# Performance work log

Hardware: AMD Instinct MI355X
Metric: run time of the kernel (lower is better)

Reference implementation:

```python
import jax, jax.numpy as jnp
import numpy as np

EPS = 1e-8
N = 1024          # number of points
C = 16            # channels per layer
RBF_LOW, RBF_HIGH, RBF_COUNT = 0.0, 3.5, 32


def _rand(key, shape, scale=0.1):
    return scale * jax.random.normal(key, shape, dtype=jnp.float32)


def setup_inputs() -> dict:
    key = jax.random.key(0)
    ks = jax.random.split(key, 20)
    R = RBF_COUNT
    return {
        'points':   jax.random.normal(ks[0], (N, 3), dtype=jnp.float32),
        # layer 1: 2 radial filters (0->0 and 0->1), output_dim = 1 input channel
        'l1_W1':    _rand(ks[1],  (2, R, R)),
        'l1_B1':    _rand(ks[2],  (2, R)),
        'l1_W2':    _rand(ks[3],  (2, R, 1)),
        'l1_B2':    _rand(ks[4],  (2, 1)),
        'l1_si0_w': _rand(ks[5],  (C, 1)),
        'l1_si0_b': _rand(ks[6],  (C,)),
        'l1_si1_w': _rand(ks[7],  (C, 1)),
        'l1_nl_b':  _rand(ks[8],  (C,)),
        # layer 2: 5 radial filters (0->0, 0->1, 1->0, 1->1 id, 1->1 levi-civita)
        'l2_W1':    _rand(ks[9],  (5, R, R)),
        'l2_B1':    _rand(ks[10], (5, R)),
        'l2_W2':    _rand(ks[11], (5, R, C)),
        'l2_B2':    _rand(ks[12], (5, C)),
        'l2_si0_w': _rand(ks[13], (C, 2 * C)),
        'l2_si0_b': _rand(ks[14], (C,)),
        'l2_si1_w': _rand(ks[15], (C, 3 * C)),
        'l2_nl_b':  _rand(ks[16], (C,)),
        # readout
        'fc_w':     _rand(ks[17], (C, 8)),
        'fc_b':     _rand(ks[18], (8,)),
    }


def _eijk():
    e = np.zeros((3, 3, 3), dtype=np.float32)
    e[0, 1, 2] = e[1, 2, 0] = e[2, 0, 1] = 1.0
    e[0, 2, 1] = e[2, 1, 0] = e[1, 0, 2] = -1.0
    return jnp.asarray(e)


def _norm_eps(x, axis, keepdims=False):
    # norm_with_epsilon: sqrt(max(sum(x^2), EPS))
    return jnp.sqrt(jnp.maximum(jnp.sum(x * x, axis=axis, keepdims=keepdims), EPS))


def _radial(rbf, w1, b1, w2, b2):
    # R(): two-layer relu MLP on rbf features -> [N, N, F]
    h = jax.nn.relu(rbf @ w1 + b1)
    return h @ w2 + b2


def _geometry(points):
    rij = points[:, None, :] - points[None, :, :]          # [N,N,3]
    ss = jnp.sum(rij * rij, axis=-1)                        # [N,N]
    mask0 = ss < EPS                                        # dij == 0 (diagonal)
    dij = jnp.where(mask0, 0.0, jnp.sqrt(jnp.where(mask0, 1.0, ss)))
    centers = jnp.linspace(RBF_LOW, RBF_HIGH, RBF_COUNT, dtype=jnp.float32)
    gamma = jnp.float32(RBF_COUNT / (RBF_HIGH - RBF_LOW))
    rbf = jnp.exp(-gamma * (dij[..., None] - centers) ** 2)  # [N,N,RBF]
    unit = rij / _norm_eps(rij, axis=-1, keepdims=True)       # unit_vectors
    return rbf, unit, mask0


def _F1(rad, unit, mask0):
    # F_1: mask radial where dij==0, multiply by unit vectors -> [N,N,F,3]
    mr = jnp.where(mask0[..., None], 0.0, rad)
    return mr[..., None] * unit[:, :, None, :]


def _nonlinearity(x0, x1, b1):
    # degree-0: pointwise elu; degree-1: norm nonlinearity x * elu(|x|+b)/|x|
    x0 = jax.nn.elu(x0)
    n = _norm_eps(x1, axis=-1)                              # [N,C]
    x1 = x1 * (jax.nn.elu(n + b1) / n)[..., None]
    return x0, x1


def reference(points, l1_W1, l1_B1, l1_W2, l1_B2, l1_si0_w, l1_si0_b, l1_si1_w,
              l1_nl_b, l2_W1, l2_B1, l2_W2, l2_B2, l2_si0_w, l2_si0_b, l2_si1_w,
              l2_nl_b, fc_w, fc_b):
    rbf, unit, mask0 = _geometry(points)
    eijk = _eijk().astype(points.dtype)
    n_pts = points.shape[0]
    x0 = jnp.ones((n_pts, 1, 1), dtype=points.dtype)        # degree-0 input [N,1,1]

    # ---- layer 1: only degree-0 input -> (0->0) and (0->1) filters ----
    r00 = _radial(rbf, l1_W1[0], l1_B1[0], l1_W2[0], l1_B2[0])
    out0 = jnp.einsum('abf,bfi->afi', r00, x0)              # filter_0
    F1a = _F1(_radial(rbf, l1_W1[1], l1_B1[1], l1_W2[1], l1_B2[1]), unit, mask0)
    out1 = jnp.einsum('abfi,bf->afi', F1a, x0[..., 0])
    x0 = jnp.einsum('afi,gf->agi', out0, l1_si0_w) + l1_si0_b[:, None]
    x1 = jnp.einsum('afi,gf->agi', out1, l1_si1_w)
    x0, x1 = _nonlinearity(x0, x1, l1_nl_b)                 # [N,C,1], [N,C,3]

    # ---- layer 2: degree-0 and degree-1 inputs -> 5 filters ----
    rads = [_radial(rbf, l2_W1[i], l2_B1[i], l2_W2[i], l2_B2[i]) for i in range(5)]
    c00 = jnp.einsum('abf,bfi->afi', rads[0], x0)                          # 0x0->0
    c01 = jnp.einsum('abfi,bf->afi', _F1(rads[1], unit, mask0), x0[..., 0])  # 0x1->1
    c10 = jnp.einsum('abfj,bfj->af', _F1(rads[2], unit, mask0), x1)[..., None]  # 1x1->0
    c11 = jnp.einsum('abf,bfi->afi', rads[3], x1)                          # 1x0->1
    c11x = jnp.einsum('ijk,abfj,bfk->afi', eijk, _F1(rads[4], unit, mask0), x1)  # 1x1->1
    cat0 = jnp.concatenate([c00, c10], axis=-2)             # [N,2C,1]
    cat1 = jnp.concatenate([c01, c11, c11x], axis=-2)       # [N,3C,3]
    x0 = jnp.einsum('afi,gf->agi', cat0, l2_si0_w) + l2_si0_b[:, None]
    x1 = jnp.einsum('afi,gf->agi', cat1, l2_si1_w)
    x0, x1 = _nonlinearity(x0, x1, l2_nl_b)

    # ---- readout: invariant degree-0 features, mean-pool over points ----
    g = jnp.mean(x0[..., 0], axis=0)                        # [C]
    return g @ fc_w + fc_b                                  # [num_classes]
```

## Files before the change

### kernel.cpp

```cpp
#include <hip/hip_runtime.h>
#include <hip/hip_bf16.h>
#include <math.h>

#define NP 1024
#define R 32
#define C 16
#define GAMMA (32.0f/3.5f)
#define DC (3.5f/31.0f)

typedef __attribute__((ext_vector_type(8))) short bf16x8;
typedef __attribute__((ext_vector_type(4))) float f32x4;

__device__ __forceinline__ short tobf(float x){
    __hip_bfloat16 h = __float2bfloat16(x);
    return __builtin_bit_cast(short, h);
}
__device__ __forceinline__ float frombf(short s){
    __hip_bfloat16 h = __builtin_bit_cast(__hip_bfloat16, s);
    return __bfloat162float(h);
}
__device__ __forceinline__ unsigned pack2bf(float a, float b){
    const unsigned lo = (unsigned short)tobf(a);
    const unsigned hi = (unsigned short)tobf(b);
    return lo | (hi << 16);
}
__device__ __forceinline__ float eluf(float x){ return x > 0.f ? x : expm1f(x); }

__device__ __forceinline__ f32x4 mfma16(bf16x8 a, bf16x8 b, f32x4 c){
    return __builtin_amdgcn_mfma_f32_16x16x32_bf16(a, b, c, 0, 0, 0);
}

template<int STRIDE>
__device__ __forceinline__ void load_bfrag(const float* __restrict__ src, int q, int n,
                                           bf16x8& hi, bf16x8& lo){
    #pragma unroll
    for (int jj = 0; jj < 8; jj++){
        const float w = src[(q*8+jj)*STRIDE + n];
        const short h = tobf(w);
        hi[jj] = h;
        lo[jj] = tobf(w - frombf(h));
    }
}

__global__ __launch_bounds__(256) void k_layer1(
    const float* __restrict__ points,
    const float* __restrict__ W1, const float* __restrict__ B1,
    const float* __restrict__ W2, const float* __restrict__ B2,
    float* __restrict__ out0, float* __restrict__ out1)
{
    __shared__ float sS0[4][32];
    __shared__ float sT[4][32][3];
    __shared__ float sUp[4][3];

    const int tid  = threadIdx.x;
    const int lane = tid & 63;
    const int wv   = tid >> 6;
    const int l16  = lane & 15;
    const int q    = lane >> 4;
    const int a    = blockIdx.x;
    const float pax = points[a*3+0], pay = points[a*3+1], paz = points[a*3+2];

    bf16x8 w1hi[2][2], w1lo[2][2];
    float  b1v[2][2];
    #pragma unroll
    for (int fi = 0; fi < 2; fi++)
        #pragma unroll
        for (int nt = 0; nt < 2; nt++){
            load_bfrag<R>(W1 + fi*R*R, q, nt*16 + l16, w1hi[fi][nt], w1lo[fi][nt]);
            b1v[fi][nt] = B1[fi*R + nt*16 + l16];
        }

    float s0a[2] = {0.f, 0.f};
    float T[2][3] = {};
    float upx = 0.f, upy = 0.f, upz = 0.f;

    for (int bt = 0; bt < 16; bt++){
        const int bA = bt*64 + wv*16 + l16;
        const float rx = pax - points[bA*3+0];
        const float ry = pay - points[bA*3+1];
        const float rz = paz - points[bA*3+2];
        const float ss = rx*rx + ry*ry + rz*rz;
        const float dij = sqrtf(ss);
        const float inv = 1.0f / sqrtf(fmaxf(ss, 1e-8f));
        const float ux = rx*inv, uy = ry*inv, uz = rz*inv;
        upx += ux; upy += uy; upz += uz;

        bf16x8 afrag;
        #pragma unroll
        for (int jj = 0; jj < 8; jj++){
            const float t = dij - (float)(q*8+jj)*DC;
            afrag[jj] = tobf(__expf(-GAMMA*t*t));
        }

        float uxr[4], uyr[4], uzr[4];
        #pragma unroll
        for (int r4 = 0; r4 < 4; r4++){
            const int sl = q*4 + r4;
            uxr[r4] = __shfl(ux, sl, 16);
            uyr[r4] = __shfl(uy, sl, 16);
            uzr[r4] = __shfl(uz, sl, 16);
        }

        #pragma unroll
        for (int nt = 0; nt < 2; nt++){
            f32x4 c = {b1v[0][nt], b1v[0][nt], b1v[0][nt], b1v[0][nt]};
            c = mfma16(afrag, w1hi[0][nt], c);
            c = mfma16(afrag, w1lo[0][nt], c);
            s0a[nt] += fmaxf(c[0],0.f)+fmaxf(c[1],0.f)+fmaxf(c[2],0.f)+fmaxf(c[3],0.f);
        }
        #pragma unroll
        for (int nt = 0; nt < 2; nt++){
            f32x4 c = {b1v[1][nt], b1v[1][nt], b1v[1][nt], b1v[1][nt]};
            c = mfma16(afrag, w1hi[1][nt], c);
            c = mfma16(afrag, w1lo[1][nt], c);
            #pragma unroll
            for (int r4 = 0; r4 < 4; r4++){
                const float h = fmaxf(c[r4], 0.f);
                T[nt][0] = fmaf(h, uxr[r4], T[nt][0]);
                T[nt][1] = fmaf(h, uyr[r4], T[nt][1]);
                T[nt][2] = fmaf(h, uzr[r4], T[nt][2]);
            }
        }
    }

    #pragma unroll
    for (int nt = 0; nt < 2; nt++){
        s0a[nt] += __shfl_down(s0a[nt], 32, 64);
        s0a[nt] += __shfl_down(s0a[nt], 16, 64);
        #pragma unroll
        for (int i = 0; i < 3; i++){
            T[nt][i] += __shfl_down(T[nt][i], 32, 64);
            T[nt][i] += __shfl_down(T[nt][i], 16, 64);
        }
    }
    #pragma unroll
    for (int off = 32; off > 0; off >>= 1){
        upx += __shfl_down(upx, off, 64);
        upy += __shfl_down(upy, off, 64);
        upz += __shfl_down(upz, off, 64);
    }
    if (lane < 16){
        sS0[wv][lane]      = s0a[0];
        sS0[wv][16 + lane] = s0a[1];
        #pragma unroll
        for (int i = 0; i < 3; i++){
            sT[wv][lane][i]      = T[0][i];
            sT[wv][16 + lane][i] = T[1][i];
        }
    }
    if (lane == 0){ sUp[wv][0] = upx; sUp[wv][1] = upy; sUp[wv][2] = upz; }
    __syncthreads();
    if (tid == 0){
        float o0 = 0.f;
        for (int j = 0; j < R; j++){
            const float S = sS0[0][j] + sS0[1][j] + sS0[2][j] + sS0[3][j];
            o0 = fmaf(S, W2[j], o0);
        }
        out0[a] = o0 + (float)NP * B2[0];
        for (int i = 0; i < 3; i++){
            float t = 0.f;
            for (int j = 0; j < R; j++){
                const float Tj = sT[0][j][i] + sT[1][j][i] + sT[2][j][i] + sT[3][j][i];
                t = fmaf(Tj, W2[R + j], t);
            }
            const float Ui = 0.25f * (sUp[0][i] + sUp[1][i] + sUp[2][i] + sUp[3][i]);
            out1[a*3+i] = t + B2[1] * Ui;
        }
    }
}

__global__ __launch_bounds__(256) void k_point1(
    const float* __restrict__ out0, const float* __restrict__ out1,
    const float* __restrict__ si0_w, const float* __restrict__ si0_b,
    const float* __restrict__ si1_w, const float* __restrict__ nl_b,
    float* __restrict__ x0g, float* __restrict__ x1s)
{
    const int b = blockIdx.x*256 + threadIdx.x;
    if (b >= NP) return;
    const float o0 = out0[b];
    const float o1x = out1[b*3+0], o1y = out1[b*3+1], o1z = out1[b*3+2];
    #pragma unroll
    for (int g = 0; g < C; g++){
        x0g[b*C+g] = eluf(fmaf(o0, si0_w[g], si0_b[g]));
        const float w = si1_w[g];
        const float tx = o1x*w, ty = o1y*w, tz = o1z*w;
        const float n = sqrtf(fmaxf(tx*tx + ty*ty + tz*tz, 1e-8f));
        const float sc = eluf(n + nl_b[g]) / n;
        x1s[0*NP*C + b*C+g] = tx*sc;
        x1s[1*NP*C + b*C+g] = ty*sc;
        x1s[2*NP*C + b*C+g] = tz*sc;
    }
}

__global__ __launch_bounds__(256) void k_layer2(
    const float* __restrict__ points,
    const float* __restrict__ W1, const float* __restrict__ B1,
    const float* __restrict__ W2, const float* __restrict__ B2,
    const float* __restrict__ x0g, const float* __restrict__ x1s,
    float* __restrict__ c00, float* __restrict__ c10)
{
    __shared__ __align__(16) short sH[4][2][16*40];
    __shared__ float sRed[4][2][16];

    const int tid  = threadIdx.x;
    const int lane = tid & 63;
    const int wv   = tid >> 6;
    const int l16  = lane & 15;
    const int q    = lane >> 4;
    const int a    = blockIdx.x;
    const float pax = points[a*3+0], pay = points[a*3+1], paz = points[a*3+2];

    bf16x8 w1hi[2][2], w1lo[2][2], w2hi[2], w2lo[2];
    float  b1v[2][2], b2v[2];
    #pragma unroll
    for (int fi = 0; fi < 2; fi++){
        const int fx = (fi == 0) ? 0 : 2;
        #pragma unroll
        for (int nt = 0; nt < 2; nt++){
            load_bfrag<R>(W1 + fx*R*R, q, 2*l16 + nt, w1hi[fi][nt], w1lo[fi][nt]);
            b1v[fi][nt] = B1[fx*R + 2*l16 + nt];
        }
        load_bfrag<C>(W2 + fx*R*C, q, l16, w2hi[fi], w2lo[fi]);
        b2v[fi] = B2[fx*C + l16];
    }

    float acc0 = 0.f, acc1 = 0.f;
    short* sH0 = sH[wv][0];
    short* sH1 = sH[wv][1];

    for (int bt = 0; bt < 16; bt++){
        const int bA = bt*64 + wv*16 + l16;
        const float rx = pax - points[bA*3+0];
        const float ry = pay - points[bA*3+1];
        const float rz = paz - points[bA*3+2];
        const float ss = rx*rx + ry*ry + rz*rz;
        const float dij = sqrtf(ss);
        const float inv = 1.0f / sqrtf(fmaxf(ss, 1e-8f));
        const float ux = rx*inv, uy = ry*inv, uz = rz*inv;

        float uxr[4], uyr[4], uzr[4];
        #pragma unroll
        for (int r4 = 0; r4 < 4; r4++){
            const int sl = q*4 + r4;
            uxr[r4] = __shfl(ux, sl, 16);
            uyr[r4] = __shfl(uy, sl, 16);
            uzr[r4] = __shfl(uz, sl, 16);
        }

        const int rb = (bt*64 + wv*16 + q*4)*C + l16;
        float x0v[4], udv[4];
        #pragma unroll
        for (int r4 = 0; r4 < 4; r4++){
            x0v[r4] = x0g[rb + r4*C];
            const float v0 = x1s[0*NP*C + rb + r4*C];
            const float v1 = x1s[1*NP*C + rb + r4*C];
            const float v2 = x1s[2*NP*C + rb + r4*C];
            udv[r4] = uxr[r4]*v0 + uyr[r4]*v1 + uzr[r4]*v2;
        }

        bf16x8 afrag;
        #pragma unroll
        for (int jj = 0; jj < 8; jj++){
            const float t = dij - (float)(q*8+jj)*DC;
            afrag[jj] = tobf(__expf(-GAMMA*t*t));
        }

        #pragma unroll
        for (int fi = 0; fi < 2; fi++){
            f32x4 c0 = {b1v[fi][0], b1v[fi][0], b1v[fi][0], b1v[fi][0]};
            c0 = mfma16(afrag, w1hi[fi][0], c0);
            c0 = mfma16(afrag, w1lo[fi][0], c0);
            f32x4 c1 = {b1v[fi][1], b1v[fi][1], b1v[fi][1], b1v[fi][1]};
            c1 = mfma16(afrag, w1hi[fi][1], c1);
            c1 = mfma16(afrag, w1lo[fi][1], c1);
            short* sHf = (fi == 0) ? sH0 : sH1;
            #pragma unroll
            for (int r4 = 0; r4 < 4; r4++){
                const unsigned p = pack2bf(fmaxf(c0[r4], 0.f), fmaxf(c1[r4], 0.f));
                *(unsigned*)&sHf[(q*4+r4)*40 + 2*l16] = p;
            }
        }
        asm volatile("s_waitcnt lgkmcnt(0)" ::: "memory");
        #pragma unroll
        for (int fi = 0; fi < 2; fi++){
            const short* sHf = (fi == 0) ? sH0 : sH1;
            const bf16x8 hf = *(const bf16x8*)(sHf + l16*40 + q*8);
            f32x4 d = {0.f, 0.f, 0.f, 0.f};
            d = mfma16(hf, w2hi[fi], d);
            d = mfma16(hf, w2lo[fi], d);
            #pragma unroll
            for (int r4 = 0; r4 < 4; r4++){
                const float v = d[r4] + b2v[fi];
                if (fi == 0) acc0 = fmaf(v, x0v[r4], acc0);
                else         acc1 = fmaf(v, udv[r4], acc1);
            }
        }
    }

    acc0 += __shfl_down(acc0, 32, 64); acc0 += __shfl_down(acc0, 16, 64);
    acc1 += __shfl_down(acc1, 32, 64); acc1 += __shfl_down(acc1, 16, 64);
    if (lane < 16){ sRed[wv][0][lane] = acc0; sRed[wv][1][lane] = acc1; }
    __syncthreads();
    if (tid < 16)
        c00[a*C + tid] = sRed[0][0][tid] + sRed[1][0][tid] + sRed[2][0][tid] + sRed[3][0][tid];
    else if (tid < 32){
        const int f = tid - 16;
        c10[a*C + f] = sRed[0][1][f] + sRed[1][1][f] + sRed[2][1][f] + sRed[3][1][f];
    }
}

__global__ __launch_bounds__(256) void k_readout1(
    const float* __restrict__ c00, const float* __restrict__ c10,
    const float* __restrict__ si0_w, const float* __restrict__ si0_b,
    float* __restrict__ partial)
{
    __shared__ float sred[4*C];
    const int tid = threadIdx.x;
    const int a = blockIdx.x*256 + tid;
    float v00[C], v10[C];
    #pragma unroll
    for (int f = 0; f < C; f++){ v00[f] = c00[a*C+f]; v10[f] = c10[a*C+f]; }
    float xg[C];
    #pragma unroll
    for (int g = 0; g < C; g++){
        float s = si0_b[g];
        #pragma unroll
        for (int f = 0; f < C; f++) s = fmaf(v00[f], si0_w[g*2*C + f], s);
        #pragma unroll
        for (int f = 0; f < C; f++) s = fmaf(v10[f], si0_w[g*2*C + C + f], s);
        xg[g] = eluf(s);
    }
    #pragma unroll
    for (int off = 32; off > 0; off >>= 1){
        #pragma unroll
        for (int g = 0; g < C; g++) xg[g] += __shfl_down(xg[g], off, 64);
    }
    const int lane = tid & 63, wv = tid >> 6;
    if (lane == 0){
        #pragma unroll
        for (int g = 0; g < C; g++) sred[wv*C + g] = xg[g];
    }
    __syncthreads();
    if (tid < C)
        partial[blockIdx.x*C + tid] =
            sred[tid] + sred[C + tid] + sred[2*C + tid] + sred[3*C + tid];
}

__global__ void k_readout2(const float* __restrict__ partial,
                           const float* __restrict__ fc_w,
                           const float* __restrict__ fc_b,
                           float* __restrict__ out)
{
    const int o = threadIdx.x;
    if (o < 8){
        float s = fc_b[o];
        #pragma unroll
        for (int g = 0; g < C; g++){
            const float m = (partial[g] + partial[C+g] + partial[2*C+g] + partial[3*C+g])
                            * (1.0f / (float)NP);
            s = fmaf(m, fc_w[g*8 + o], s);
        }
        out[o] = s;
    }
}

extern "C" void kernel_launch(void* const* d_in, const int* in_sizes, int n_in,
                              void* d_out, int out_size, void* d_ws, size_t ws_size,
                              hipStream_t stream)
{
    (void)in_sizes; (void)n_in; (void)out_size; (void)ws_size;
    const float* points   = (const float*)d_in[0];
    const float* l1_W1    = (const float*)d_in[1];
    const float* l1_B1    = (const float*)d_in[2];
    const float* l1_W2    = (const float*)d_in[3];
    const float* l1_B2    = (const float*)d_in[4];
    const float* l1_si0_w = (const float*)d_in[5];
    const float* l1_si0_b = (const float*)d_in[6];
    const float* l1_si1_w = (const float*)d_in[7];
    const float* l1_nl_b  = (const float*)d_in[8];
    const float* l2_W1    = (const float*)d_in[9];
    const float* l2_B1    = (const float*)d_in[10];
    const float* l2_W2    = (const float*)d_in[11];
    const float* l2_B2    = (const float*)d_in[12];
    const float* l2_si0_w = (const float*)d_in[13];
    const float* l2_si0_b = (const float*)d_in[14];
    const float* fc_w     = (const float*)d_in[17];
    const float* fc_b     = (const float*)d_in[18];

    float* ws      = (float*)d_ws;
    float* out0    = ws;
    float* out1    = out0 + NP;
    float* x0g     = out1 + NP*3;
    float* x1s     = x0g + NP*C;
    float* c00     = x1s + 3*NP*C;
    float* c10     = c00 + NP*C;
    float* partial = c10 + NP*C;

    k_layer1<<<NP, 256, 0, stream>>>(points, l1_W1, l1_B1, l1_W2, l1_B2, out0, out1);
    k_point1<<<NP/256, 256, 0, stream>>>(out0, out1, l1_si0_w, l1_si0_b, l1_si1_w, l1_nl_b, x0g, x1s);
    k_layer2<<<NP, 256, 0, stream>>>(points, l2_W1, l2_B1, l2_W2, l2_B2, x0g, x1s, c00, c10);
    k_readout1<<<NP/256, 256, 0, stream>>>(c00, c10, l2_si0_w, l2_si0_b, partial);
    k_readout2<<<1, 64, 0, stream>>>(partial, fc_w, fc_b, (float*)d_out);
}
```

Baseline: 173.4 us.

## Split pairwise kernels over two neighbor halves and streamline bf16 conversion

Both pairwise layer kernels now launch two blocks per point, each covering half of the neighbor range, and write partial sums that the following pointwise kernels add together. This doubles the block count from 1024 to 2048 to improve CU occupancy and tail balance. In exchange, each block reloads the weight fragments and there are extra partial-buffer writes and reads. The bf16 conversion is replaced by manual round-to-nearest bit arithmetic with packed pair construction for the RBF fragment. The second-layer bias is also folded into the MFMA accumulator init.

```diff
diff --git a/kernel.cpp b/kernel.cpp
--- a/kernel.cpp
+++ b/kernel.cpp
@@ -10,24 +10,37 @@
 
 typedef __attribute__((ext_vector_type(8))) short bf16x8;
 typedef __attribute__((ext_vector_type(4))) float f32x4;
-
+typedef __attribute__((ext_vector_type(4))) unsigned u32x4;
+
+__device__ __forceinline__ unsigned bfbits(float x){
+    unsigned u = __builtin_bit_cast(unsigned, x);
+    return u + 0x7FFFu + ((u >> 16) & 1u);
+}
 __device__ __forceinline__ short tobf(float x){
-    __hip_bfloat16 h = __float2bfloat16(x);
-    return __builtin_bit_cast(short, h);
+    return (short)(bfbits(x) >> 16);
 }
 __device__ __forceinline__ float frombf(short s){
-    __hip_bfloat16 h = __builtin_bit_cast(__hip_bfloat16, s);
-    return __bfloat162float(h);
+    const unsigned u = ((unsigned)(unsigned short)s) << 16;
+    return __builtin_bit_cast(float, u);
 }
 __device__ __forceinline__ unsigned pack2bf(float a, float b){
-    const unsigned lo = (unsigned short)tobf(a);
-    const unsigned hi = (unsigned short)tobf(b);
-    return lo | (hi << 16);
+    return (bfbits(a) >> 16) | (bfbits(b) & 0xFFFF0000u);
 }
 __device__ __forceinline__ float eluf(float x){ return x > 0.f ? x : expm1f(x); }
 
 __device__ __forceinline__ f32x4 mfma16(bf16x8 a, bf16x8 b, f32x4 c){
     return __builtin_amdgcn_mfma_f32_16x16x32_bf16(a, b, c, 0, 0, 0);
+}
+
+__device__ __forceinline__ bf16x8 make_afrag(float dij, int q){
+    u32x4 av;
+    #pragma unroll
+    for (int p = 0; p < 4; p++){
+        const float t0 = dij - (float)(q*8 + 2*p)*DC;
+        const float t1 = dij - (float)(q*8 + 2*p + 1)*DC;
+        av[p] = pack2bf(__expf(-GAMMA*t0*t0), __expf(-GAMMA*t1*t1));
+    }
+    return __builtin_bit_cast(bf16x8, av);
 }
 
 template<int STRIDE>
@@ -46,7 +59,7 @@
     const float* __restrict__ points,
     const float* __restrict__ W1, const float* __restrict__ B1,
     const float* __restrict__ W2, const float* __restrict__ B2,
-    float* __restrict__ out0, float* __restrict__ out1)
+    float* __restrict__ out0h, float* __restrict__ out1h)
 {
     __shared__ float sS0[4][32];
     __shared__ float sT[4][32][3];
@@ -57,7 +70,8 @@
     const int wv   = tid >> 6;
     const int l16  = lane & 15;
     const int q    = lane >> 4;
-    const int a    = blockIdx.x;
+    const int a    = blockIdx.x >> 1;
+    const int half = blockIdx.x & 1;
     const float pax = points[a*3+0], pay = points[a*3+1], paz = points[a*3+2];
 
     bf16x8 w1hi[2][2], w1lo[2][2];
@@ -74,7 +88,7 @@
     float T[2][3] = {};
     float upx = 0.f, upy = 0.f, upz = 0.f;
 
-    for (int bt = 0; bt < 16; bt++){
+    for (int bt = half*8; bt < half*8 + 8; bt++){
         const int bA = bt*64 + wv*16 + l16;
         const float rx = pax - points[bA*3+0];
         const float ry = pay - points[bA*3+1];
@@ -85,12 +99,7 @@
         const float ux = rx*inv, uy = ry*inv, uz = rz*inv;
         upx += ux; upy += uy; upz += uz;
 
-        bf16x8 afrag;
-        #pragma unroll
-        for (int jj = 0; jj < 8; jj++){
-            const float t = dij - (float)(q*8+jj)*DC;
-            afrag[jj] = tobf(__expf(-GAMMA*t*t));
-        }
+        const bf16x8 afrag = make_afrag(dij, q);
 
         float uxr[4], uyr[4], uzr[4];
         #pragma unroll
@@ -156,7 +165,7 @@
             const float S = sS0[0][j] + sS0[1][j] + sS0[2][j] + sS0[3][j];
             o0 = fmaf(S, W2[j], o0);
         }
-        out0[a] = o0 + (float)NP * B2[0];
+        out0h[half*NP + a] = o0 + (float)(NP/2) * B2[0];
         for (int i = 0; i < 3; i++){
             float t = 0.f;
             for (int j = 0; j < R; j++){
@@ -164,21 +173,23 @@
                 t = fmaf(Tj, W2[R + j], t);
             }
             const float Ui = 0.25f * (sUp[0][i] + sUp[1][i] + sUp[2][i] + sUp[3][i]);
-            out1[a*3+i] = t + B2[1] * Ui;
+            out1h[(half*NP + a)*3 + i] = t + B2[1] * Ui;
         }
     }
 }
 
 __global__ __launch_bounds__(256) void k_point1(
-    const float* __restrict__ out0, const float* __restrict__ out1,
+    const float* __restrict__ out0h, const float* __restrict__ out1h,
     const float* __restrict__ si0_w, const float* __restrict__ si0_b,
     const float* __restrict__ si1_w, const float* __restrict__ nl_b,
     float* __restrict__ x0g, float* __restrict__ x1s)
 {
     const int b = blockIdx.x*256 + threadIdx.x;
     if (b >= NP) return;
-    const float o0 = out0[b];
-    const float o1x = out1[b*3+0], o1y = out1[b*3+1], o1z = out1[b*3+2];
+    const float o0 = out0h[b] + out0h[NP + b];
+    const float o1x = out1h[b*3+0] + out1h[(NP+b)*3+0];
+    const float o1y = out1h[b*3+1] + out1h[(NP+b)*3+1];
+    const float o1z = out1h[b*3+2] + out1h[(NP+b)*3+2];
     #pragma unroll
     for (int g = 0; g < C; g++){
         x0g[b*C+g] = eluf(fmaf(o0, si0_w[g], si0_b[g]));
@@ -197,7 +208,7 @@
     const float* __restrict__ W1, const float* __restrict__ B1,
     const float* __restrict__ W2, const float* __restrict__ B2,
     const float* __restrict__ x0g, const float* __restrict__ x1s,
-    float* __restrict__ c00, float* __restrict__ c10)
+    float* __restrict__ c00h, float* __restrict__ c10h)
 {
     __shared__ __align__(16) short sH[4][2][16*40];
     __shared__ float sRed[4][2][16];
@@ -207,7 +218,8 @@
     const int wv   = tid >> 6;
     const int l16  = lane & 15;
     const int q    = lane >> 4;
-    const int a    = blockIdx.x;
+    const int a    = blockIdx.x >> 1;
+    const int half = blockIdx.x & 1;
     const float pax = points[a*3+0], pay = points[a*3+1], paz = points[a*3+2];
 
     bf16x8 w1hi[2][2], w1lo[2][2], w2hi[2], w2lo[2];
@@ -228,7 +240,7 @@
     short* sH0 = sH[wv][0];
     short* sH1 = sH[wv][1];
 
-    for (int bt = 0; bt < 16; bt++){
+    for (int bt = half*8; bt < half*8 + 8; bt++){
         const int bA = bt*64 + wv*16 + l16;
         const float rx = pax - points[bA*3+0];
         const float ry = pay - points[bA*3+1];
@@ -258,12 +270,7 @@
             udv[r4] = uxr[r4]*v0 + uyr[r4]*v1 + uzr[r4]*v2;
         }
 
-        bf16x8 afrag;
-        #pragma unroll
-        for (int jj = 0; jj < 8; jj++){
-            const float t = dij - (float)(q*8+jj)*DC;
-            afrag[jj] = tobf(__expf(-GAMMA*t*t));
-        }
+        const bf16x8 afrag = make_afrag(dij, q);
 
         #pragma unroll
         for (int fi = 0; fi < 2; fi++){
@@ -285,14 +292,13 @@
         for (int fi = 0; fi < 2; fi++){
             const short* sHf = (fi == 0) ? sH0 : sH1;
             const bf16x8 hf = *(const bf16x8*)(sHf + l16*40 + q*8);
-            f32x4 d = {0.f, 0.f, 0.f, 0.f};
+            f32x4 d = {b2v[fi], b2v[fi], b2v[fi], b2v[fi]};
             d = mfma16(hf, w2hi[fi], d);
             d = mfma16(hf, w2lo[fi], d);
             #pragma unroll
             for (int r4 = 0; r4 < 4; r4++){
-                const float v = d[r4] + b2v[fi];
-                if (fi == 0) acc0 = fmaf(v, x0v[r4], acc0);
-                else         acc1 = fmaf(v, udv[r4], acc1);
+                if (fi == 0) acc0 = fmaf(d[r4], x0v[r4], acc0);
+                else         acc1 = fmaf(d[r4], udv[r4], acc1);
             }
         }
     }
@@ -302,15 +308,17 @@
     if (lane < 16){ sRed[wv][0][lane] = acc0; sRed[wv][1][lane] = acc1; }
     __syncthreads();
     if (tid < 16)
-        c00[a*C + tid] = sRed[0][0][tid] + sRed[1][0][tid] + sRed[2][0][tid] + sRed[3][0][tid];
+        c00h[half*NP*C + a*C + tid] =
+            sRed[0][0][tid] + sRed[1][0][tid] + sRed[2][0][tid] + sRed[3][0][tid];
     else if (tid < 32){
         const int f = tid - 16;
-        c10[a*C + f] = sRed[0][1][f] + sRed[1][1][f] + sRed[2][1][f] + sRed[3][1][f];
+        c10h[half*NP*C + a*C + f] =
+            sRed[0][1][f] + sRed[1][1][f] + sRed[2][1][f] + sRed[3][1][f];
     }
 }
 
 __global__ __launch_bounds__(256) void k_readout1(
-    const float* __restrict__ c00, const float* __restrict__ c10,
+    const float* __restrict__ c00h, const float* __restrict__ c10h,
     const float* __restrict__ si0_w, const float* __restrict__ si0_b,
     float* __restrict__ partial)
 {
@@ -319,7 +327,10 @@
     const int a = blockIdx.x*256 + tid;
     float v00[C], v10[C];
     #pragma unroll
-    for (int f = 0; f < C; f++){ v00[f] = c00[a*C+f]; v10[f] = c10[a*C+f]; }
+    for (int f = 0; f < C; f++){
+        v00[f] = c00h[a*C+f] + c00h[NP*C + a*C+f];
+        v10[f] = c10h[a*C+f] + c10h[NP*C + a*C+f];
+    }
     float xg[C];
     #pragma unroll
     for (int g = 0; g < C; g++){
@@ -388,17 +399,17 @@
     const float* fc_b     = (const float*)d_in[18];
 
     float* ws      = (float*)d_ws;
-    float* out0    = ws;
-    float* out1    = out0 + NP;
-    float* x0g     = out1 + NP*3;
+    float* out0h   = ws;
+    float* out1h   = out0h + 2*NP;
+    float* x0g     = out1h + 2*NP*3;
     float* x1s     = x0g + NP*C;
-    float* c00     = x1s + 3*NP*C;
-    float* c10     = c00 + NP*C;
-    float* partial = c10 + NP*C;
-
-    k_layer1<<<NP, 256, 0, stream>>>(points, l1_W1, l1_B1, l1_W2, l1_B2, out0, out1);
-    k_point1<<<NP/256, 256, 0, stream>>>(out0, out1, l1_si0_w, l1_si0_b, l1_si1_w, l1_nl_b, x0g, x1s);
-    k_layer2<<<NP, 256, 0, stream>>>(points, l2_W1, l2_B1, l2_W2, l2_B2, x0g, x1s, c00, c10);
-    k_readout1<<<NP/256, 256, 0, stream>>>(c00, c10, l2_si0_w, l2_si0_b, partial);
+    float* c00h    = x1s + 3*NP*C;
+    float* c10h    = c00h + 2*NP*C;
+    float* partial = c10h + 2*NP*C;
+
+    k_layer1<<<2*NP, 256, 0, stream>>>(points, l1_W1, l1_B1, l1_W2, l1_B2, out0h, out1h);
+    k_point1<<<NP/256, 256, 0, stream>>>(out0h, out1h, l1_si0_w, l1_si0_b, l1_si1_w, l1_nl_b, x0g, x1s);
+    k_layer2<<<2*NP, 256, 0, stream>>>(points, l2_W1, l2_B1, l2_W2, l2_B2, x0g, x1s, c00h, c10h);
+    k_readout1<<<NP/256, 256, 0, stream>>>(c00h, c10h, l2_si0_w, l2_si0_b, partial);
     k_readout2<<<1, 64, 0, stream>>>(partial, fc_w, fc_b, (float*)d_out);
 }
```

After: 186.6 us. 1.08x slower.
